# Kernel optimization log

Hardware: AMD Instinct MI355X
Metric: run time of the kernel (lower is better)

Reference implementation:

```python
import jax, jax.numpy as jnp
import numpy as np
from jax import lax

EPS = 1e-4  # BatchNorm2d eps
K, STRIDE, PAD = 3, 1, 1


def _conv_nchw(x, w, stride, pad):
    return lax.conv_general_dilated(
        x, w, window_strides=(stride, stride), padding=[(pad, pad), (pad, pad)],
        dimension_numbers=("NCHW", "OIHW", "NCHW"))


def setup_inputs() -> dict:
    key = jax.random.key(0)
    ks = jax.random.split(key, 6)
    N, C, H, W = 16, 256, 56, 56
    Cout = 256
    return {
        "x": jax.random.normal(ks[0], (N, C, H, W), jnp.float32),
        "bn_gamma": jax.random.uniform(ks[1], (C,), jnp.float32, 0.5, 1.5),
        "bn_beta": jax.random.normal(ks[2], (C,), jnp.float32) * 0.1,
        "conv_w": jax.random.normal(ks[3], (Cout, C, K, K), jnp.float32) * (1.0 / np.sqrt(C * K * K)),
        "conv_b": jax.random.normal(ks[4], (Cout,), jnp.float32) * 0.01,
        "beta_conv_b": jax.random.normal(ks[5], (1,), jnp.float32) * 0.01,
    }


def reference(x, bn_gamma, bn_beta, conv_w, conv_b, beta_conv_b):
    # --- BatchNorm2d (training-mode batch stats, affine) ---
    mean = jnp.mean(x, axis=(0, 2, 3), keepdims=True)
    var = jnp.mean(jnp.square(x - mean), axis=(0, 2, 3), keepdims=True)  # biased
    xn = (x - mean) * lax.rsqrt(var + EPS)
    xn = xn * bn_gamma[None, :, None, None] + bn_beta[None, :, None, None]

    # --- Ternary quantize (threshold=0; le overwrites ge, so x==0 -> -1) ---
    t = jnp.where(xn >= 0.0, 1.0, 0.0)
    t = jnp.where(xn <= 0.0, -1.0, t).astype(xn.dtype)
    # scale=True, clamp=True
    xc = jnp.clip(xn, -1.0, 1.0)
    c_sum = jnp.sum(xc * t, axis=1, keepdims=True)       # [N,1,H,W]
    c_cnt = jnp.sum(jnp.abs(t), axis=1, keepdims=True)   # L1 norm over channels

    # --- Main conv on ternary activations ---
    y = _conv_nchw(t, conv_w, STRIDE, PAD) + conv_b[None, :, None, None]

    # --- beta: ones-weight box filter (+ beta_conv bias) ---
    ones_k = jnp.ones((1, 1, K, K), x.dtype)
    b_sum = _conv_nchw(c_sum, ones_k, STRIDE, PAD) + beta_conv_b[0]
    b_cnt = _conv_nchw(c_cnt, ones_k, STRIDE, PAD) + beta_conv_b[0]
    beta_map = b_sum / b_cnt                             # [N,1,Ho,Wo]
    return y * beta_map
```

## Files before the change

kernel.cpp:

```cpp
#include <hip/hip_runtime.h>
#include <hip/hip_bf16.h>

typedef __attribute__((ext_vector_type(8))) short bf16x8;
typedef __attribute__((ext_vector_type(4))) float f32x4;

#define NB 16
#define C 256
#define HH 56
#define WW 56
#define HW 3136
#define CHW 802816
#define NPIX 50176
#define PH 58
#define PW 58
#define KTOT 2304
#define PPI 3364
#define NPIXP 53824

#define GLL(g, l) __builtin_amdgcn_global_load_lds( \
    (const __attribute__((address_space(1))) void*)(g), \
    (__attribute__((address_space(3))) void*)(l), 16, 0, 0)

__global__ __launch_bounds__(1024) void prep_stats_kernel(const float* __restrict__ x,
                             const float* __restrict__ gamma, const float* __restrict__ cw,
                             double* __restrict__ stats, unsigned short* __restrict__ Wp,
                             unsigned short* __restrict__ Tp, float* __restrict__ csum) {
  int b = blockIdx.x, tid = threadIdx.x;
  if (b < 256) {
    int c = b;
    double s = 0.0, s2 = 0.0;
    const float* xc = x + (size_t)c * HW;
    for (int k = tid; k < NB * (HW / 4); k += 1024) {
      int n = k / (HW / 4), i = k - n * (HW / 4);
      float4 v = *(const float4*)(xc + (size_t)n * CHW + i * 4);
      double a = v.x, bb = v.y, cc = v.z, d = v.w;
      s  += (a + bb) + (cc + d);
      s2 += (a * a + bb * bb) + (cc * cc + d * d);
    }
    __shared__ double rs[1024], rq[1024];
    rs[tid] = s; rq[tid] = s2; __syncthreads();
    for (int o = 512; o > 0; o >>= 1) {
      if (tid < o) { rs[tid] += rs[tid + o]; rq[tid] += rq[tid + o]; }
      __syncthreads();
    }
    if (tid == 0) {
      double mean = rs[0] / (double)NPIX;
      double var = rq[0] / (double)NPIX - mean * mean;
      stats[c] = mean;
      stats[C + c] = (double)gamma[c] / sqrt(var + 1e-4);
    }
  } else if (b < 320) {
    int co = (b - 256) * 4 + (tid >> 8);
    int c  = tid & 255;
    const float* src = cw + (size_t)co * KTOT + c * 9;
    int p = (c & 31) * 8 + (c >> 5);
    int ck = p >> 5, v = p & 31;
    int quad = v >> 3, j = v & 7;
    int cb = co >> 4, row16 = co & 15;
    int lane8 = (quad * 16 + row16) * 8 + j;
#pragma unroll
    for (int tap = 0; tap < 9; ++tap) {
      unsigned u = __builtin_bit_cast(unsigned, src[tap]);
      unsigned lsb = (u >> 16) & 1u;
      u += 0x7FFFu + lsb;
      Wp[(size_t)(((ck * 9 + tap) * 16) + cb) * 512 + lane8] = (unsigned short)(u >> 16);
    }
  } else if (b < 434) {
    int g = (b - 320) * 1024 + tid;
    int n = g / 7296; int r = g - n * 7296;
    int pix = r >> 5, c8 = r & 31;
    int h, w;
    if (pix < 58)      { h = 0;  w = pix; }
    else if (pix < 116){ h = 57; w = pix - 58; }
    else { int rem = pix - 116; h = 1 + (rem >> 1); w = (rem & 1) ? 57 : 0; }
    uint4 z = {0u, 0u, 0u, 0u};
    *(uint4*)(Tp + (size_t)((n * PH + h) * PW + w) * C + c8 * 8) = z;
  } else {
    int i = (b - 434) * 1024 + tid;
    if (i < NPIXP) csum[i] = 0.f;
  }
}

__global__ __launch_bounds__(256) void ternarize_kernel(const float* __restrict__ x,
                                 const float* __restrict__ beta,
                                 const double* __restrict__ stats,
                                 unsigned short* __restrict__ Tp, float* __restrict__ csum) {
  int bid = blockIdx.x, tid = threadIdx.x;
  int n = bid / HH, h = bid - n * HH;
  __shared__ float xs[256][57];
  const float* xb = x + (size_t)n * CHW + h * WW;
#pragma unroll
  for (int j = 0; j < 14; ++j) {
    int idx = j * 256 + tid;
    int c = idx / 14, q = idx - c * 14;
    float4 v = *(const float4*)(xb + (size_t)c * HW + q * 4);
    float* row = &xs[c][q * 4];
    row[0] = v.x; row[1] = v.y; row[2] = v.z; row[3] = v.w;
  }
  int c8 = tid & 31;
  double mu[8], sc[8], bt[8];
#pragma unroll
  for (int e = 0; e < 8; ++e) {
    int c = c8 + 32 * e;
    mu[e] = stats[c]; sc[e] = stats[C + c]; bt[e] = (double)beta[c];
  }
  __syncthreads();
  unsigned short* tb = Tp + ((size_t)(n * PH + h + 1) * PW + 1) * C;
  float* cs = csum + (size_t)(n * PH + h + 1) * PW + 1;
#pragma unroll
  for (int p = 0; p < 7; ++p) {
    int idx = p * 256 + tid;
    int w = idx >> 5;
    unsigned bits[4];
    float msum = 0.f;
#pragma unroll
    for (int e2 = 0; e2 < 4; ++e2) {
      unsigned lo, hi;
      {
        double xn = ((double)xs[c8 + 64 * e2][w] - mu[2 * e2]) * sc[2 * e2] + bt[2 * e2];
        lo = (xn > 0.0) ? 0x3F80u : 0xBF80u;
        msum += (float)fmin(fabs(xn), 1.0);
      }
      {
        double xn = ((double)xs[c8 + 64 * e2 + 32][w] - mu[2 * e2 + 1]) * sc[2 * e2 + 1] + bt[2 * e2 + 1];
        hi = (xn > 0.0) ? 0x3F80u : 0xBF80u;
        msum += (float)fmin(fabs(xn), 1.0);
      }
      bits[e2] = lo | (hi << 16);
    }
    msum += __shfl_xor(msum, 1); msum += __shfl_xor(msum, 2);
    msum += __shfl_xor(msum, 4); msum += __shfl_xor(msum, 8);
    msum += __shfl_xor(msum, 16);
    uint4 v4; v4.x = bits[0]; v4.y = bits[1]; v4.z = bits[2]; v4.w = bits[3];
    *(uint4*)(tb + (size_t)w * C + c8 * 8) = v4;
    if (c8 == 0) cs[w] = msum;
  }
}

__global__ __launch_bounds__(256, 2) void conv_kernel(const unsigned short* __restrict__ Wp,
    const unsigned short* __restrict__ Tp, const float* __restrict__ convb,
    const float* __restrict__ csum, const float* __restrict__ betab,
    float* __restrict__ out) {
  int bid = blockIdx.x;
  int ptg = bid >> 5, xcd = bid & 7, ct = (bid >> 3) & 3;
  int pt = ptg * 8 + xcd;
  if (pt >= 211) return;
  int tid = threadIdx.x;

  __shared__ __align__(16) unsigned short Bs[2][384 * 32];

  int wstart = pt * 256 - 59;
  int bofs[6];
#pragma unroll
  for (int r = 0; r < 6; ++r) {
    int lin = r * 256 + tid;
    int bpix = lin >> 2, pseg = lin & 3;
    int lseg = pseg ^ ((bpix >> 1) & 3);
    int q = wstart + bpix;
    q = q < 0 ? 0 : (q >= NPIXP ? NPIXP - 1 : q);
    bofs[r] = q * C + lseg * 8;
  }

  int lane = tid & 63, wid = tid >> 6;
  int quad = lane >> 4, row16 = lane & 15;
  int pixb = wid * 64 + row16;

  const bf16x8* Ab = (const bf16x8*)Wp + lane;
  int cb0 = ct * 4;

  f32x4 acc[4][4];
#pragma unroll
  for (int mi = 0; mi < 4; ++mi)
#pragma unroll
    for (int ni = 0; ni < 4; ++ni)
      acc[mi][ni] = (f32x4){0.f, 0.f, 0.f, 0.f};

#pragma unroll
  for (int r = 0; r < 6; ++r) GLL(Tp + bofs[r], &Bs[0][(r * 256 + tid) * 8]);

  for (int ck = 0; ck < 8; ++ck) {
    int cur = ck & 1;
    __syncthreads();
    if (ck < 7) {
      int c2 = (ck + 1) * 32;
#pragma unroll
      for (int r = 0; r < 6; ++r) GLL(Tp + bofs[r] + c2, &Bs[cur ^ 1][(r * 256 + tid) * 8]);
    }
    const unsigned short* bB = &Bs[cur][0];
    __builtin_amdgcn_s_setprio(1);
#pragma unroll
    for (int kh = 0; kh < 3; ++kh) {
      bf16x8 a[3][4];
#pragma unroll
      for (int kw = 0; kw < 3; ++kw)
#pragma unroll
        for (int mi = 0; mi < 4; ++mi)
          a[kw][mi] = Ab[(size_t)(((ck * 9 + kh * 3 + kw) * 16) + cb0 + mi) * 64];
#pragma unroll
      for (int kw = 0; kw < 3; ++kw) {
        bf16x8 b[4];
#pragma unroll
        for (int ni = 0; ni < 4; ++ni) {
          int pix = pixb + ni * 16 + kh * 58 + kw;
          b[ni] = *(const bf16x8*)(bB + pix * 32 + ((quad ^ ((pix >> 1) & 3)) * 8));
        }
#pragma unroll
        for (int mi = 0; mi < 4; ++mi)
#pragma unroll
          for (int ni = 0; ni < 4; ++ni)
            acc[mi][ni] = __builtin_amdgcn_mfma_f32_16x16x32_bf16(a[kw][mi], b[ni], acc[mi][ni], 0, 0, 0);
      }
    }
    __builtin_amdgcn_s_setprio(0);
  }

  int co0 = ct * 64;
  float bb = betab[0];
#pragma unroll
  for (int ni = 0; ni < 4; ++ni) {
    int pp = pt * 256 + wid * 64 + ni * 16 + row16;
    if (pp >= NPIXP) continue;
    int n = pp / PPI; int r2 = pp - n * PPI;
    int ph = r2 / PW;  int pw = r2 - ph * PW;
    if (ph < 1 || ph > 56 || pw < 1 || pw > 56) continue;
    const float* cp = csum + (size_t)(n * PH + ph - 1) * PW + (pw - 1);
    float s9 = 0.f;
#pragma unroll
    for (int i = 0; i < 3; ++i)
#pragma unroll
      for (int j = 0; j < 3; ++j) s9 += cp[i * PW + j];
    int rows = 3 - (ph == 1) - (ph == 56);
    int cols = 3 - (pw == 1) - (pw == 56);
    float bm = (s9 + bb) / (256.0f * (float)(rows * cols) + bb);
    int pix = (ph - 1) * WW + (pw - 1);
    float* ob = out + (size_t)n * CHW + pix;
#pragma unroll
    for (int mi = 0; mi < 4; ++mi) {
      int co = co0 + mi * 16 + quad * 4;
#pragma unroll
      for (int rg = 0; rg < 4; ++rg) {
        ob[(size_t)(co + rg) * HW] = (acc[mi][ni][rg] + convb[co + rg]) * bm;
      }
    }
  }
}

extern "C" void kernel_launch(void* const* d_in, const int* in_sizes, int n_in,
                              void* d_out, int out_size, void* d_ws, size_t ws_size,
                              hipStream_t stream) {
  const float* x     = (const float*)d_in[0];
  const float* gamma = (const float*)d_in[1];
  const float* beta  = (const float*)d_in[2];
  const float* convw = (const float*)d_in[3];
  const float* convb = (const float*)d_in[4];
  const float* betab = (const float*)d_in[5];
  float* out = (float*)d_out;

  char* ws = (char*)d_ws;
  unsigned short* Tp   = (unsigned short*)(ws);
  unsigned short* Wp   = (unsigned short*)(ws + 27557888);
  float*          csum = (float*)(ws + 28737536);
  double*         stats= (double*)(ws + 29153536);

  prep_stats_kernel<<<487, 1024, 0, stream>>>(x, gamma, convw, stats, Wp, Tp, csum);
  ternarize_kernel<<<896, 256, 0, stream>>>(x, beta, stats, Tp, csum);
  conv_kernel<<<864, 256, 0, stream>>>(Wp, Tp, convb, csum, betab, out);
}
```

Before: 233.9 us.

## Split K loop into per-kh stages with smaller LDS tile and register-prefetched weights

Restructures the implicit-GEMM conv main loop from 8 channel chunks (each loading a 384-pixel halo tile covering all three kernel rows) into 24 stages indexed by (kh, channel chunk). Each stage loads only a 320-pixel strip for one kernel row, and the weight fragments for the next stage are prefetched into a second register set. The aim is to cut LDS footprint and hide weight-load latency behind the MFMA work. In exchange it issues more barriers and global-to-LDS loads in total, since rows are reloaded once per kh, and it raises register pressure from the two 12-entry fragment arrays.

```diff
diff --git a/kernel.cpp b/kernel.cpp
--- a/kernel.cpp
+++ b/kernel.cpp
@@ -147,24 +147,25 @@
   if (pt >= 211) return;
   int tid = threadIdx.x;
 
-  __shared__ __align__(16) unsigned short Bs[2][384 * 32];
-
-  int wstart = pt * 256 - 59;
-  int bofs[6];
-#pragma unroll
-  for (int r = 0; r < 6; ++r) {
+  __shared__ __align__(16) unsigned short Bs[2][320 * 32];
+
+  int bofs3[3][5];
+#pragma unroll
+  for (int r = 0; r < 5; ++r) {
     int lin = r * 256 + tid;
-    int bpix = lin >> 2, pseg = lin & 3;
-    int lseg = pseg ^ ((bpix >> 1) & 3);
-    int q = wstart + bpix;
-    q = q < 0 ? 0 : (q >= NPIXP ? NPIXP - 1 : q);
-    bofs[r] = q * C + lseg * 8;
+    int bpix = lin >> 2;
+    int bl = (lin & 3) ^ ((bpix >> 1) & 3);
+#pragma unroll
+    for (int kh = 0; kh < 3; ++kh) {
+      int q = pt * 256 + (kh - 1) * 58 - 32 + bpix;
+      q = q < 0 ? 0 : (q >= NPIXP ? NPIXP - 1 : q);
+      bofs3[kh][r] = q * C + bl * 8;
+    }
   }
 
   int lane = tid & 63, wid = tid >> 6;
   int quad = lane >> 4, row16 = lane & 15;
-  int pixb = wid * 64 + row16;
-
+  int jbase = wid * 64 + row16 + 31;
   const bf16x8* Ab = (const bf16x8*)Wp + lane;
   int cb0 = ct * 4;
 
@@ -175,44 +176,57 @@
     for (int ni = 0; ni < 4; ++ni)
       acc[mi][ni] = (f32x4){0.f, 0.f, 0.f, 0.f};
 
-#pragma unroll
-  for (int r = 0; r < 6; ++r) GLL(Tp + bofs[r], &Bs[0][(r * 256 + tid) * 8]);
-
-  for (int ck = 0; ck < 8; ++ck) {
-    int cur = ck & 1;
-    __syncthreads();
-    if (ck < 7) {
-      int c2 = (ck + 1) * 32;
-#pragma unroll
-      for (int r = 0; r < 6; ++r) GLL(Tp + bofs[r] + c2, &Bs[cur ^ 1][(r * 256 + tid) * 8]);
-    }
-    const unsigned short* bB = &Bs[cur][0];
-    __builtin_amdgcn_s_setprio(1);
-#pragma unroll
-    for (int kh = 0; kh < 3; ++kh) {
-      bf16x8 a[3][4];
-#pragma unroll
-      for (int kw = 0; kw < 3; ++kw)
-#pragma unroll
-        for (int mi = 0; mi < 4; ++mi)
-          a[kw][mi] = Ab[(size_t)(((ck * 9 + kh * 3 + kw) * 16) + cb0 + mi) * 64];
-#pragma unroll
-      for (int kw = 0; kw < 3; ++kw) {
-        bf16x8 b[4];
-#pragma unroll
-        for (int ni = 0; ni < 4; ++ni) {
-          int pix = pixb + ni * 16 + kh * 58 + kw;
-          b[ni] = *(const bf16x8*)(bB + pix * 32 + ((quad ^ ((pix >> 1) & 3)) * 8));
-        }
-#pragma unroll
-        for (int mi = 0; mi < 4; ++mi)
-#pragma unroll
-          for (int ni = 0; ni < 4; ++ni)
-            acc[mi][ni] = __builtin_amdgcn_mfma_f32_16x16x32_bf16(a[kw][mi], b[ni], acc[mi][ni], 0, 0, 0);
-      }
-    }
-    __builtin_amdgcn_s_setprio(0);
-  }
+  bf16x8 aA[12], aB[12];
+
+#pragma unroll
+  for (int r = 0; r < 5; ++r) GLL(Tp + bofs3[0][r], &Bs[0][(r * 256 + tid) * 8]);
+#pragma unroll
+  for (int t3 = 0; t3 < 3; ++t3)
+#pragma unroll
+    for (int mi = 0; mi < 4; ++mi)
+      aA[t3 * 4 + mi] = Ab[(cb0 + t3 * 16 + mi) * 64];
+
+#define STAGE(S, ACUR, ANEXT, PREF)                                              \
+  {                                                                              \
+    __syncthreads();       \
+    if (PREF) {                                                                  \
+      int s2 = (S) + 1; int kh2 = s2 >> 3; int c2 = (s2 & 7) * 32;               \
+      _Pragma("unroll")                                                          \
+      for (int r = 0; r < 5; ++r)                                                \
+        GLL(Tp + bofs3[kh2][r] + c2, &Bs[s2 & 1][(r * 256 + tid) * 8]);          \
+      int fb = (((s2 & 7) * 9 + kh2 * 3) * 16 + cb0) * 64;                       \
+      _Pragma("unroll")                                                          \
+      for (int t3 = 0; t3 < 3; ++t3)                                             \
+        _Pragma("unroll")                                                        \
+        for (int mi = 0; mi < 4; ++mi)                                           \
+          ANEXT[t3 * 4 + mi] = Ab[fb + (t3 * 16 + mi) * 64];                     \
+    }                                                                            \
+    const unsigned short* bB = &Bs[(S) & 1][0];                                  \
+    __builtin_amdgcn_s_setprio(1);                                               \
+    _Pragma("unroll")                                                            \
+    for (int kw = 0; kw < 3; ++kw) {                                             \
+      bf16x8 bfr[4];                                                             \
+      _Pragma("unroll")                                                          \
+      for (int ni = 0; ni < 4; ++ni) {                                           \
+        int pix = jbase + ni * 16 + kw;                                          \
+        bfr[ni] = *(const bf16x8*)(bB + pix * 32 + ((quad ^ ((pix >> 1) & 3)) * 8)); \
+      }                                                                          \
+      _Pragma("unroll")                                                          \
+      for (int mi = 0; mi < 4; ++mi)                                             \
+        _Pragma("unroll")                                                        \
+        for (int ni = 0; ni < 4; ++ni)                                           \
+          acc[mi][ni] = __builtin_amdgcn_mfma_f32_16x16x32_bf16(                 \
+              ACUR[kw * 4 + mi], bfr[ni], acc[mi][ni], 0, 0, 0);                 \
+    }                                                                            \
+    __builtin_amdgcn_s_setprio(0);                                               \
+  }
+
+  for (int sp = 0; sp < 12; ++sp) {
+    int s0 = 2 * sp;
+    STAGE(s0, aA, aB, 1);
+    STAGE(s0 + 1, aB, aA, (sp < 11));
+  }
+#undef STAGE
 
   int co0 = ct * 64;
   float bb = betab[0];
```

After: 201.9 us. -13.7%, faster.

## Restructure conv into 256-channel tiles with LDS-staged weights and tap-level pipelining

Applied to the files above, without the earlier changes.

The conv kernel now uses 512-thread blocks that each compute all 256 output channels for a 256-pixel tile, instead of four blocks per pixel tile each covering 64 channels. Weights are repacked into a plain [co][tap][c] bf16 layout and streamed into double-buffered LDS per tap via global_load_lds. Activation chunks of 64 channels are prefetched mid-loop, with explicit vmcnt waits and barriers. This is meant to stop re-reading activations four times and to replace direct global weight loads with LDS reuse. The cost is far fewer blocks (211 on a large GPU), so the device may be underutilised, plus higher register and LDS use per block.

```diff
diff --git a/kernel.cpp b/kernel.cpp
--- a/kernel.cpp
+++ b/kernel.cpp
@@ -53,17 +53,14 @@
     int co = (b - 256) * 4 + (tid >> 8);
     int c  = tid & 255;
     const float* src = cw + (size_t)co * KTOT + c * 9;
+    unsigned short* dst = Wp + (size_t)co * KTOT;
     int p = (c & 31) * 8 + (c >> 5);
-    int ck = p >> 5, v = p & 31;
-    int quad = v >> 3, j = v & 7;
-    int cb = co >> 4, row16 = co & 15;
-    int lane8 = (quad * 16 + row16) * 8 + j;
-#pragma unroll
-    for (int tap = 0; tap < 9; ++tap) {
-      unsigned u = __builtin_bit_cast(unsigned, src[tap]);
+#pragma unroll
+    for (int t9 = 0; t9 < 9; ++t9) {
+      unsigned u = __builtin_bit_cast(unsigned, src[t9]);
       unsigned lsb = (u >> 16) & 1u;
       u += 0x7FFFu + lsb;
-      Wp[(size_t)(((ck * 9 + tap) * 16) + cb) * 512 + lane8] = (unsigned short)(u >> 16);
+      dst[t9 * 256 + p] = (unsigned short)(u >> 16);
     }
   } else if (b < 434) {
     int g = (b - 320) * 1024 + tid;
@@ -137,88 +134,113 @@
   }
 }
 
-__global__ __launch_bounds__(256, 2) void conv_kernel(const unsigned short* __restrict__ Wp,
+__global__ __launch_bounds__(512, 2) void conv_kernel(const unsigned short* __restrict__ Wp,
     const unsigned short* __restrict__ Tp, const float* __restrict__ convb,
     const float* __restrict__ csum, const float* __restrict__ betab,
     float* __restrict__ out) {
-  int bid = blockIdx.x;
-  int ptg = bid >> 5, xcd = bid & 7, ct = (bid >> 3) & 3;
-  int pt = ptg * 8 + xcd;
-  if (pt >= 211) return;
+  int pt = blockIdx.x;
   int tid = threadIdx.x;
 
-  __shared__ __align__(16) unsigned short Bs[2][384 * 32];
-
+  __shared__ __align__(16) unsigned short Abuf[2][16384];
+  __shared__ __align__(16) unsigned short Bbuf[2][24576];
+
+  int aofs[4];
+#pragma unroll
+  for (int r = 0; r < 4; ++r) {
+    int lin = r * 512 + tid;
+    int half = lin >> 10, ks = (lin >> 9) & 1, co127 = (lin >> 2) & 127, pseg = lin & 3;
+    int lseg = pseg ^ ((co127 >> 1) & 3);
+    aofs[r] = (half * 128 + co127) * KTOT + ks * 32 + lseg * 8;
+  }
   int wstart = pt * 256 - 59;
   int bofs[6];
 #pragma unroll
   for (int r = 0; r < 6; ++r) {
-    int lin = r * 256 + tid;
-    int bpix = lin >> 2, pseg = lin & 3;
-    int lseg = pseg ^ ((bpix >> 1) & 3);
-    int q = wstart + bpix;
+    int ks = (r >= 3);
+    int row = ((r - ks * 3) * 512 + tid) >> 2;
+    int pseg = tid & 3;
+    int lseg = pseg ^ ((row >> 1) & 3);
+    int q = wstart + row;
     q = q < 0 ? 0 : (q >= NPIXP ? NPIXP - 1 : q);
-    bofs[r] = q * C + lseg * 8;
+    bofs[r] = q * C + ks * 32 + lseg * 8;
   }
 
   int lane = tid & 63, wid = tid >> 6;
+  int wr = wid >> 2, wc = wid & 3;
   int quad = lane >> 4, row16 = lane & 15;
-  int pixb = wid * 64 + row16;
-
-  const bf16x8* Ab = (const bf16x8*)Wp + lane;
-  int cb0 = ct * 4;
-
-  f32x4 acc[4][4];
-#pragma unroll
-  for (int mi = 0; mi < 4; ++mi)
+  int aRd = wr * 8192 + row16 * 32 + (quad ^ ((row16 >> 1) & 3)) * 8;
+  int wcr = wc * 64 + row16;
+
+  f32x4 acc[8][4];
+#pragma unroll
+  for (int mi = 0; mi < 8; ++mi)
 #pragma unroll
     for (int ni = 0; ni < 4; ++ni)
       acc[mi][ni] = (f32x4){0.f, 0.f, 0.f, 0.f};
 
-#pragma unroll
-  for (int r = 0; r < 6; ++r) GLL(Tp + bofs[r], &Bs[0][(r * 256 + tid) * 8]);
-
-  for (int ck = 0; ck < 8; ++ck) {
-    int cur = ck & 1;
-    __syncthreads();
-    if (ck < 7) {
-      int c2 = (ck + 1) * 32;
-#pragma unroll
-      for (int r = 0; r < 6; ++r) GLL(Tp + bofs[r] + c2, &Bs[cur ^ 1][(r * 256 + tid) * 8]);
-    }
-    const unsigned short* bB = &Bs[cur][0];
-    __builtin_amdgcn_s_setprio(1);
-#pragma unroll
-    for (int kh = 0; kh < 3; ++kh) {
-      bf16x8 a[3][4];
-#pragma unroll
-      for (int kw = 0; kw < 3; ++kw)
-#pragma unroll
-        for (int mi = 0; mi < 4; ++mi)
-          a[kw][mi] = Ab[(size_t)(((ck * 9 + kh * 3 + kw) * 16) + cb0 + mi) * 64];
-#pragma unroll
-      for (int kw = 0; kw < 3; ++kw) {
-        bf16x8 b[4];
-#pragma unroll
-        for (int ni = 0; ni < 4; ++ni) {
-          int pix = pixb + ni * 16 + kh * 58 + kw;
-          b[ni] = *(const bf16x8*)(bB + pix * 32 + ((quad ^ ((pix >> 1) & 3)) * 8));
-        }
-#pragma unroll
-        for (int mi = 0; mi < 4; ++mi)
+  {
+    unsigned short* bd = &Bbuf[0][0] + tid * 8;
+#pragma unroll
+    for (int r = 0; r < 6; ++r) GLL(Tp + bofs[r], bd + r * 4096);
+    unsigned short* ad = &Abuf[0][0] + tid * 8;
+#pragma unroll
+    for (int r = 0; r < 4; ++r) GLL(Wp + aofs[r], ad + r * 4096);
+  }
+
+  for (int cc = 0; cc < 4; ++cc) {
+    for (int tap = 0; tap < 9; ++tap) {
+      int s = cc * 9 + tap;
+      __builtin_amdgcn_sched_barrier(0);
+      __builtin_amdgcn_s_barrier();
+      __builtin_amdgcn_sched_barrier(0);
+      if (s < 35) {
+        int ntap = (tap == 8) ? 0 : tap + 1;
+        int ncc  = (tap == 8) ? cc + 1 : cc;
+        int aadd = ntap * 256 + ncc * 64;
+        unsigned short* ad = &Abuf[(s + 1) & 1][0] + tid * 8;
+#pragma unroll
+        for (int r = 0; r < 4; ++r) GLL(Wp + aofs[r] + aadd, ad + r * 4096);
+      }
+      if (tap == 6 && cc < 3) {
+        int badd = (cc + 1) * 64;
+        unsigned short* bd = &Bbuf[(cc + 1) & 1][0] + tid * 8;
+#pragma unroll
+        for (int r = 0; r < 6; ++r) GLL(Tp + bofs[r] + badd, bd + r * 4096);
+      }
+      if (s == 35)                                 asm volatile("s_waitcnt vmcnt(0)" ::: "memory");
+      else if ((tap == 6 || tap == 7) && cc < 3)   asm volatile("s_waitcnt vmcnt(10)" ::: "memory");
+      else                                         asm volatile("s_waitcnt vmcnt(4)" ::: "memory");
+      __builtin_amdgcn_s_barrier();
+      __builtin_amdgcn_sched_barrier(0);
+      int kh = tap / 3;
+      int rbase = wcr + tap + 55 * kh;
+      int bsw = (quad ^ ((rbase >> 1) & 3)) * 8;
+      const unsigned short* aB = &Abuf[s & 1][0] + aRd;
+      const unsigned short* bB = &Bbuf[cc & 1][0] + rbase * 32 + bsw;
+#pragma unroll
+      for (int ks = 0; ks < 2; ++ks) {
+        bf16x8 a[8], b[4];
+#pragma unroll
+        for (int mi = 0; mi < 8; ++mi)
+          a[mi] = *(const bf16x8*)(aB + ks * 4096 + mi * 512);
+#pragma unroll
+        for (int ni = 0; ni < 4; ++ni)
+          b[ni] = *(const bf16x8*)(bB + ks * 12288 + ni * 512);
+        __builtin_amdgcn_s_setprio(1);
+#pragma unroll
+        for (int mi = 0; mi < 8; ++mi)
 #pragma unroll
           for (int ni = 0; ni < 4; ++ni)
-            acc[mi][ni] = __builtin_amdgcn_mfma_f32_16x16x32_bf16(a[kw][mi], b[ni], acc[mi][ni], 0, 0, 0);
-      }
-    }
-    __builtin_amdgcn_s_setprio(0);
-  }
-
-  int co0 = ct * 64;
+            acc[mi][ni] = __builtin_amdgcn_mfma_f32_16x16x32_bf16(a[mi], b[ni], acc[mi][ni], 0, 0, 0);
+        __builtin_amdgcn_s_setprio(0);
+      }
+    }
+  }
+
   float bb = betab[0];
 #pragma unroll
   for (int ni = 0; ni < 4; ++ni) {
-    int pp = pt * 256 + wid * 64 + ni * 16 + row16;
+    int pp = pt * 256 + wc * 64 + ni * 16 + row16;
     if (pp >= NPIXP) continue;
     int n = pp / PPI; int r2 = pp - n * PPI;
     int ph = r2 / PW;  int pw = r2 - ph * PW;
@@ -235,8 +257,8 @@
     int pix = (ph - 1) * WW + (pw - 1);
     float* ob = out + (size_t)n * CHW + pix;
 #pragma unroll
-    for (int mi = 0; mi < 4; ++mi) {
-      int co = co0 + mi * 16 + quad * 4;
+    for (int mi = 0; mi < 8; ++mi) {
+      int co = wr * 128 + mi * 16 + quad * 4;
 #pragma unroll
       for (int rg = 0; rg < 4; ++rg) {
         ob[(size_t)(co + rg) * HW] = (acc[mi][ni][rg] + convb[co + rg]) * bm;
@@ -264,5 +286,5 @@
 
   prep_stats_kernel<<<487, 1024, 0, stream>>>(x, gamma, convw, stats, Wp, Tp, csum);
   ternarize_kernel<<<896, 256, 0, stream>>>(x, beta, stats, Tp, csum);
-  conv_kernel<<<864, 256, 0, stream>>>(Wp, Tp, convb, csum, betab, out);
-}
+  conv_kernel<<<211, 512, 0, stream>>>(Wp, Tp, convb, csum, betab, out);
+}
```

Result: faster. 218.7 us (-6.5%).
